# Optimization experiments

Hardware: AMD Instinct MI355X
Metric: run time of the kernel (lower is better)

## Reference

```python
import jax, jax.numpy as jnp
import numpy as np

RNN = 64

def linear(x, W, b):
    return x @ W.T + b

def sample_logprob(key, logits):
    # Categorical(softmax(logits)): sample + log_prob of the sample
    s = jax.random.categorical(key, logits)
    lp = jnp.take_along_axis(jax.nn.log_softmax(logits, -1), s[:, None], 1)[:, 0]
    return s, lp

def lstm_encode(inst, embed, W_ih, W_hh, b_ih, b_hh):
    # torch.nn.LSTMCell unrolled over the sequence; gate order i,f,g,o
    x = embed[inst]                              # [B,S,64]
    B = inst.shape[0]
    def step(carry, xt):
        h, c = carry
        gates = xt @ W_ih.T + b_ih + h @ W_hh.T + b_hh   # [B,256]
        i, f, g, o = jnp.split(gates, 4, axis=-1)
        c = jax.nn.sigmoid(f) * c + jax.nn.sigmoid(i) * jnp.tanh(g)
        h = jax.nn.sigmoid(o) * jnp.tanh(c)
        return (h, c), None
    h0 = jnp.zeros((B, RNN), x.dtype)
    (h, _), _ = jax.lax.scan(step, (h0, h0), jnp.swapaxes(x, 0, 1))
    return h

def setup_inputs():
    key = jax.random.key(0)
    ks = jax.random.split(key, 20)
    B, S, V = 16384, 32, 1000
    def nrm(k, shape, scale=0.05):
        return jax.random.normal(k, shape, jnp.float32) * scale
    return {
        "inst0": jax.random.randint(ks[0], (B, S), 0, V + 1),
        "inst1": jax.random.randint(ks[1], (B, S), 0, V + 1),
        "canvas0": jax.random.randint(ks[2], (B, 25, 4), 0, 5).astype(jnp.int32),
        "canvas1": jax.random.randint(ks[3], (B, 25, 4), 0, 5).astype(jnp.int32),
        "ref": jax.random.randint(ks[4], (B, 4), 0, 5).astype(jnp.int32),
        "embed": nrm(ks[5], (V + 1, RNN)),
        "W_ih": nrm(ks[6], (4 * RNN, RNN)), "W_hh": nrm(ks[7], (4 * RNN, RNN)),
        "b_ih": jnp.zeros(4 * RNN), "b_hh": jnp.zeros(4 * RNN),
        "Wc": nrm(ks[8], (3, RNN)), "bc": jnp.zeros(3),
        "Ws": nrm(ks[9], (3, RNN)), "bs": jnp.zeros(3),
        "Wl": nrm(ks[10], (25, RNN)), "bl": jnp.zeros(25),
        "Wr1": nrm(ks[11], (32, RNN + 4)), "br1": jnp.zeros(32),
        "Wr2": nrm(ks[12], (1, 32)), "br2": jnp.zeros(1),
        "Wp": nrm(ks[13], (8, RNN)), "bp": jnp.zeros(8),
    }

def reference(inst0, inst1, canvas0, canvas1, ref, embed, W_ih, W_hh, b_ih, b_hh,
              Wc, bc, Ws, bs, Wl, bl, Wr1, br1, Wr2, br2, Wp, bp):
    B = inst0.shape[0]
    kk = jax.random.split(jax.random.key(42), 7)
    final_canvas = canvas1                                   # [B,25,4]

    def step_rewards(loc_predict, color_sample, shape_sample):
        valid = (loc_predict >= 0) & (loc_predict < 25)
        pt = jnp.take_along_axis(final_canvas,
                                 jnp.clip(loc_predict, 0, 24)[:, None, None],
                                 axis=1)[:, 0]               # [B,4]
        ok = valid & (pt.sum(-1) >= 0)
        loc_r = jnp.where(ok, 1.0, -1.0)
        col_r = jnp.where(ok, jnp.where(color_sample == pt[:, 0], 1.0, -1.0), 0.0)
        shp_r = jnp.where(ok, jnp.where(shape_sample == pt[:, 1], 1.0, -1.0), 0.0)
        return loc_r, col_r, shp_r

    # ---- dialog step 0: absolute location ----
    h0 = lstm_encode(inst0, embed, W_ih, W_hh, b_ih, b_hh)
    cs0, clp0 = sample_logprob(kk[0], linear(h0, Wc, bc))
    ss0, slp0 = sample_logprob(kk[1], linear(h0, Ws, bs))
    loc0, llp0 = sample_logprob(kk[2], linear(h0, Wl, bl))
    loc_r0, col_r0, _ = step_rewards(loc0, cs0, ss0)

    # ---- dialog step 1: relative location w.r.t. attended ref object ----
    h1 = lstm_encode(inst1, embed, W_ih, W_hh, b_ih, b_hh)
    cs1, clp1 = sample_logprob(kk[3], linear(h1, Wc, bc))
    ss1, slp1 = sample_logprob(kk[4], linear(h1, Ws, bs))
    ls1, llp1 = sample_logprob(kk[5], linear(h1, Wp, bp))    # 8-way offset
    prev = canvas0.astype(h1.dtype)                          # [B,25,4]
    feat = jnp.concatenate([jnp.broadcast_to(h1[:, None, :], (B, 25, RNN)), prev], 2)  # [B,25,68]
    att_logits = (jax.nn.relu(feat @ Wr1.T + br1) @ Wr2.T + br2)[:, :, 0]              # [B,25]
    att_sample, alp1 = sample_logprob(kk[6], att_logits)
    ref_obj = jnp.take_along_axis(canvas0, att_sample[:, None, None], axis=1)[:, 0]    # [B,4]
    att_reward = ((ref_obj == ref).sum(-1) == 4).astype(jnp.float32) * 2.0 - 1.0
    offsets = jnp.array([[-1, 0], [1, 0], [0, 1], [0, -1],
                         [-1, -1], [-1, 1], [1, -1], [1, 1]], jnp.int32)
    off = offsets[ls1]
    loc1 = (ref_obj[:, 2] + off[:, 0]) * 5 + (ref_obj[:, 3] + off[:, 1])
    loc_r1, col_r1, _ = step_rewards(loc1, cs1, ss1)

    logp = jnp.stack([clp0, slp0, llp0, clp1, slp1, llp1, alp1])          # [7,B]
    # NB: original appends step_loc_reward into shape_rewards (kept verbatim)
    rew = jnp.stack([loc_r0, col_r0, loc_r0, loc_r1, col_r1, loc_r1, att_reward])  # [7,B]
    return logp, rew
```

## Files before the change

### kernel.cpp

```cpp
#include <hip/hip_runtime.h>
#include <hip/hip_bf16.h>
#include <stdint.h>
#include <math.h>

#define NB 16384
#define NSEQ 32
#define NV 1001
#define NROWS 32768

#define CHK 272
#define RTG (8 * CHK)
#define SPL (8 * RTG)
#define HBUF (3 * SPL)

typedef __attribute__((ext_vector_type(8))) short bf16x8;
typedef __attribute__((ext_vector_type(4))) float f32x4;

__device__ __forceinline__ void tf2x32(uint32_t k0, uint32_t k1,
                                       uint32_t x0, uint32_t x1,
                                       uint32_t& o0, uint32_t& o1) {
  const uint32_t ks0 = k0, ks1 = k1, ks2 = k0 ^ k1 ^ 0x1BD11BDAu;
  x0 += ks0; x1 += ks1;
  const int rA[4] = {13, 15, 26, 6};
  const int rB[4] = {17, 29, 16, 24};
#pragma unroll
  for (int i = 0; i < 4; ++i) { x0 += x1; x1 = (x1 << rA[i]) | (x1 >> (32 - rA[i])); x1 ^= x0; }
  x0 += ks1; x1 += ks2 + 1u;
#pragma unroll
  for (int i = 0; i < 4; ++i) { x0 += x1; x1 = (x1 << rB[i]) | (x1 >> (32 - rB[i])); x1 ^= x0; }
  x0 += ks2; x1 += ks0 + 2u;
#pragma unroll
  for (int i = 0; i < 4; ++i) { x0 += x1; x1 = (x1 << rA[i]) | (x1 >> (32 - rA[i])); x1 ^= x0; }
  x0 += ks0; x1 += ks1 + 3u;
#pragma unroll
  for (int i = 0; i < 4; ++i) { x0 += x1; x1 = (x1 << rB[i]) | (x1 >> (32 - rB[i])); x1 ^= x0; }
  x0 += ks1; x1 += ks2 + 4u;
#pragma unroll
  for (int i = 0; i < 4; ++i) { x0 += x1; x1 = (x1 << rA[i]) | (x1 >> (32 - rA[i])); x1 ^= x0; }
  o0 = x0 + ks2; o1 = x1 + ks0 + 5u;
}

__device__ __forceinline__ float gumbel_from_bits(uint32_t bits) {
  uint32_t fb = (bits >> 9) | 0x3f800000u;
  float u = __uint_as_float(fb) - 1.0f;
  u = fmaxf(u, 1.17549435e-38f);
  return -logf(-logf(u));
}

__device__ __forceinline__ float sigm(float x) { return 1.0f / (1.0f + __expf(-x)); }
__device__ __forceinline__ float tanh_(float x) {
  float e = __expf(2.0f * x);
  return 1.0f - 2.0f / (e + 1.0f);
}

__device__ __forceinline__ float dot64(const float* __restrict__ w, const float* h) {
  float a = 0.f;
#pragma unroll
  for (int k = 0; k < 64; ++k) a = fmaf(w[k], h[k], a);
  return a;
}

__device__ __forceinline__ unsigned short bfbits(float x, float& xf) {
  __hip_bfloat16 hb = __float2bfloat16(x);
  xf = __bfloat162float(hb);
  unsigned short u;
  __builtin_memcpy(&u, &hb, 2);
  return u;
}

template <int N>
__device__ __forceinline__ void samp_team(const float* lg, int g, int C,
                                          uint32_t k0, uint32_t k1, int b,
                                          int& sOut, float& lpOut) {
  float m = -__builtin_inff();
#pragma unroll
  for (int i = 0; i < N; ++i) m = fmaxf(m, lg[i]);
  m = fmaxf(m, __shfl_xor(m, 1));
  m = fmaxf(m, __shfl_xor(m, 2));
  float se = 0.f;
#pragma unroll
  for (int i = 0; i < N; ++i) se += expf(lg[i] - m);
  se += __shfl_xor(se, 1);
  se += __shfl_xor(se, 2);
  const float lse = logf(se);
  float bz = -__builtin_inff(), bl = 0.f;
  int bi = 0x7fffffff;
#pragma unroll
  for (int i = 0; i < N; ++i) {
    const int c = g + 4 * i;
    uint32_t o0, o1; tf2x32(k0, k1, 0u, (uint32_t)(b * C + c), o0, o1);
    const float z = lg[i] + gumbel_from_bits(o0 ^ o1);
    if (z > bz || (z == bz && c < bi)) { bz = z; bi = c; bl = lg[i]; }
  }
#pragma unroll
  for (int d = 1; d <= 2; d <<= 1) {
    const float z2 = __shfl_xor(bz, d);
    const int i2 = __shfl_xor(bi, d);
    const float l2 = __shfl_xor(bl, d);
    if (z2 > bz || (z2 == bz && i2 < bi)) { bz = z2; bi = i2; bl = l2; }
  }
  sOut = bi;
  lpOut = (bl - m) - lse;
}

__global__ __launch_bounds__(256) void k_prep(
    const float* __restrict__ embed, const float* __restrict__ W_ih,
    const float* __restrict__ W_hh, const float* __restrict__ b_ih,
    const float* __restrict__ b_hh, float* __restrict__ embedWi,
    unsigned short* __restrict__ Wsp) {
  if (blockIdx.x >= NV) {
    int idx = (blockIdx.x - NV) * 256 + threadIdx.x;
    int s = idx >> 14;
    int rem = idx & 16383;
    int jp = rem >> 6, m = rem & 63;
    int kc = m >> 5, q = (m >> 3) & 3, p = m & 7;
    int k = kc * 32 + q * 8 + ((p >> 1) + ((p & 1) << 2));
    int j = (jp & 3) * 64 + (jp >> 2);
    float w = W_hh[j * 64 + k];
    float f1, f2, f3;
    unsigned short b1 = bfbits(w, f1);
    unsigned short b2 = bfbits(w - f1, f2);
    unsigned short b3 = bfbits(w - f1 - f2, f3);
    Wsp[idx] = (s == 0) ? b1 : (s == 1) ? b2 : b3;
    return;
  }
  __shared__ float er[64];
  int v = blockIdx.x;
  if (threadIdx.x < 64) er[threadIdx.x] = embed[v * 64 + threadIdx.x];
  __syncthreads();
  int jp = threadIdx.x;
  int j = (jp & 3) * 64 + (jp >> 2);
  float a = b_ih[j] + b_hh[j];
#pragma unroll
  for (int k = 0; k < 64; ++k) a = fmaf(W_ih[j * 64 + k], er[k], a);
  embedWi[v * 256 + jp] = a;
}

__global__ __launch_bounds__(512, 2) void k_lstm(
    const int* __restrict__ inst0, const int* __restrict__ inst1,
    const float* __restrict__ embedWi, const unsigned short* __restrict__ Wsp,
    float* __restrict__ hT) {
  extern __shared__ char smc[];
  int* idsb = (int*)(smc + 2 * HBUF);

  const int tid = threadIdx.x;
  const int lane = tid & 63;
  const int wave = tid >> 6;
  const int wgj = wave >> 1;
  const int wrh = wave & 1;
  const int n15 = lane & 15;
  const int quad = lane >> 4;
  const int blk = blockIdx.x;
  const int rowbase = blk * 128;
  const int rb = rowbase & (NB - 1);
  const int* __restrict__ inst = (blk < 128) ? inst0 : inst1;

  bf16x8 afr[4][2][3];
#pragma unroll
  for (int jt = 0; jt < 4; ++jt) {
    const int jrow = (wgj * 4 + jt) * 16 + n15;
#pragma unroll
    for (int kc = 0; kc < 2; ++kc)
#pragma unroll
      for (int s = 0; s < 3; ++s)
        afr[jt][kc][s] =
            *(const bf16x8*)(Wsp + ((s * 256 + jrow) * 64 + kc * 32 + quad * 8));
  }
#pragma unroll
  for (int jt = 0; jt < 4; ++jt)
#pragma unroll
    for (int kc = 0; kc < 2; ++kc)
#pragma unroll
      for (int s = 0; s < 3; ++s)
        asm volatile("" : "+v"(afr[jt][kc][s]));

  for (int i = tid; i < HBUF / 4; i += 512) ((float*)smc)[i] = 0.f;
  if (tid < 128) idsb[tid] = inst[(rb + tid) * NSEQ];

  float cst[16];
#pragma unroll
  for (int i = 0; i < 16; ++i) cst[i] = 0.f;

  __syncthreads();

#pragma unroll 1
  for (int t = 0; t < NSEQ; ++t) {
    const char* __restrict__ hbr = smc + (t & 1) * HBUF;
    char* __restrict__ hbw = smc + ((t & 1) ^ 1) * HBUF;

    int vv[4];
#pragma unroll
    for (int rt = 0; rt < 4; ++rt)
      vv[rt] = idsb[(t & 1) * 128 + wrh * 64 + rt * 16 + n15];
    if (tid < 128 && t + 1 < NSEQ)
      idsb[((t + 1) & 1) * 128 + tid] = inst[(rb + tid) * NSEQ + t + 1];

    f32x4 C[4][4];
#pragma unroll
    for (int jt = 0; jt < 4; ++jt)
#pragma unroll
      for (int rt = 0; rt < 4; ++rt) C[jt][rt] = (f32x4){0.f, 0.f, 0.f, 0.f};

#pragma unroll
    for (int rt = 0; rt < 4; ++rt) {
      const int rtg = wrh * 4 + rt;
      bf16x8 bfr[2][3];
#pragma unroll
      for (int kc = 0; kc < 2; ++kc)
#pragma unroll
        for (int s = 0; s < 3; ++s)
          bfr[kc][s] = *(const bf16x8*)(hbr + s * SPL + rtg * RTG +
                                        (kc * 4 + quad) * CHK + n15 * 16);
#pragma unroll
      for (int jt = 0; jt < 4; ++jt) {
#pragma unroll
        for (int kc = 0; kc < 2; ++kc) {
          f32x4 acc = C[jt][rt];
          acc = __builtin_amdgcn_mfma_f32_16x16x32_bf16(afr[jt][kc][1], bfr[kc][2], acc, 0, 0, 0);
          acc = __builtin_amdgcn_mfma_f32_16x16x32_bf16(afr[jt][kc][2], bfr[kc][1], acc, 0, 0, 0);
          acc = __builtin_amdgcn_mfma_f32_16x16x32_bf16(afr[jt][kc][0], bfr[kc][2], acc, 0, 0, 0);
          acc = __builtin_amdgcn_mfma_f32_16x16x32_bf16(afr[jt][kc][2], bfr[kc][0], acc, 0, 0, 0);
          acc = __builtin_amdgcn_mfma_f32_16x16x32_bf16(afr[jt][kc][1], bfr[kc][1], acc, 0, 0, 0);
          acc = __builtin_amdgcn_mfma_f32_16x16x32_bf16(afr[jt][kc][0], bfr[kc][1], acc, 0, 0, 0);
          acc = __builtin_amdgcn_mfma_f32_16x16x32_bf16(afr[jt][kc][1], bfr[kc][0], acc, 0, 0, 0);
          acc = __builtin_amdgcn_mfma_f32_16x16x32_bf16(afr[jt][kc][0], bfr[kc][0], acc, 0, 0, 0);
          C[jt][rt] = acc;
        }
      }
    }

    const bool last = (t == NSEQ - 1);
    float4 esA[4], esB[4];
#pragma unroll
    for (int jt = 0; jt < 4; ++jt)
      esA[jt] = *(const float4*)(embedWi + vv[0] * 256 + (wgj * 16 + jt * 4 + quad) * 4);
#pragma unroll
    for (int rt = 0; rt < 4; ++rt) {
      if (rt < 3) {
#pragma unroll
        for (int jt = 0; jt < 4; ++jt)
          esB[jt] = *(const float4*)(embedWi + vv[rt + 1] * 256 +
                                     (wgj * 16 + jt * 4 + quad) * 4);
      }
      const int r = wrh * 64 + rt * 16 + n15;
      const int rtg = wrh * 4 + rt;
      float hval[4];
      unsigned short s1[4], s2[4], s3[4];
#pragma unroll
      for (int jt = 0; jt < 4; ++jt) {
        const float gi = C[jt][rt].x + esA[jt].x;
        const float gf = C[jt][rt].y + esA[jt].y;
        const float gg = C[jt][rt].z + esA[jt].z;
        const float go = C[jt][rt].w + esA[jt].w;
        const float ci = sigm(gf) * cst[jt * 4 + rt] + sigm(gi) * tanh_(gg);
        cst[jt * 4 + rt] = ci;
        const float h = sigm(go) * tanh_(ci);
        hval[jt] = h;
        float f1, f2, f3;
        s1[jt] = bfbits(h, f1);
        s2[jt] = bfbits(h - f1, f2);
        s3[jt] = bfbits(h - f1 - f2, f3);
      }
      char* base = hbw + rtg * RTG + n15 * 16 + quad * 4;
      *(uint32_t*)(base + 0 * SPL + (wgj * 2 + 0) * CHK) = (uint32_t)s1[0] | ((uint32_t)s1[1] << 16);
      *(uint32_t*)(base + 0 * SPL + (wgj * 2 + 1) * CHK) = (uint32_t)s1[2] | ((uint32_t)s1[3] << 16);
      *(uint32_t*)(base + 1 * SPL + (wgj * 2 + 0) * CHK) = (uint32_t)s2[0] | ((uint32_t)s2[1] << 16);
      *(uint32_t*)(base + 1 * SPL + (wgj * 2 + 1) * CHK) = (uint32_t)s2[2] | ((uint32_t)s2[3] << 16);
      *(uint32_t*)(base + 2 * SPL + (wgj * 2 + 0) * CHK) = (uint32_t)s3[0] | ((uint32_t)s3[1] << 16);
      *(uint32_t*)(base + 2 * SPL + (wgj * 2 + 1) * CHK) = (uint32_t)s3[2] | ((uint32_t)s3[3] << 16);
      if (last) {
#pragma unroll
        for (int jt = 0; jt < 4; ++jt)
          hT[(wgj * 16 + jt * 4 + quad) * NROWS + rowbase + r] = hval[jt];
      }
#pragma unroll
      for (int jt = 0; jt < 4; ++jt) esA[jt] = esB[jt];
    }
    __syncthreads();
  }
}

__global__ __launch_bounds__(256) void k_heads(
    const int* __restrict__ canvas0, const int* __restrict__ canvas1,
    const int* __restrict__ ref,
    const float* __restrict__ Wc, const float* __restrict__ bc,
    const float* __restrict__ Ws, const float* __restrict__ bs,
    const float* __restrict__ Wl, const float* __restrict__ bl,
    const float* __restrict__ Wr1, const float* __restrict__ br1,
    const float* __restrict__ Wr2, const float* __restrict__ br2,
    const float* __restrict__ Wp, const float* __restrict__ bp,
    const float* __restrict__ hT, float* __restrict__ out) {
  const int tid = threadIdx.x;
  const int g = tid & 3;
  const int s = blockIdx.x & 1;
  const int b = (blockIdx.x >> 1) * 64 + (tid >> 2);
  const float NEG = -__builtin_inff();

  uint32_t kk0[7], kk1[7];
#pragma unroll
  for (int i = 0; i < 7; ++i) {
    uint32_t o0, o1; tf2x32(0u, 42u, 0u, (uint32_t)i, o0, o1);
    kk0[i] = o0; kk1[i] = o1;
  }

  float h[64];
#pragma unroll
  for (int u = 0; u < 64; ++u) h[u] = hT[u * NROWS + s * NB + b];

  float lgc[1], lgs[1];
  lgc[0] = (g < 3) ? (bc[g] + dot64(Wc + g * 64, h)) : NEG;
  lgs[0] = (g < 3) ? (bs[g] + dot64(Ws + g * 64, h)) : NEG;

  if (s == 0) {
    int cs0, ss0, loc0; float clp0, slp0, llp0;
    samp_team<1>(lgc, g, 3, kk0[0], kk1[0], b, cs0, clp0);
    samp_team<1>(lgs, g, 3, kk0[1], kk1[1], b, ss0, slp0);
    float lgl[7];
#pragma unroll
    for (int i = 0; i < 7; ++i) {
      const int cc = g + 4 * i;
      lgl[i] = (cc < 25) ? (bl[cc] + dot64(Wl + cc * 64, h)) : NEG;
    }
    samp_team<7>(lgl, g, 25, kk0[2], kk1[2], b, loc0, llp0);

    if (g == 0) {
      const int p0 = min(max(loc0, 0), 24);
      const int4 pt = ((const int4*)(canvas1 + b * 100))[p0];
      const bool ok0 = (loc0 >= 0) && (loc0 < 25) && (pt.x + pt.y + pt.z + pt.w >= 0);
      const float loc_r0 = ok0 ? 1.f : -1.f;
      const float col_r0 = ok0 ? ((cs0 == pt.x) ? 1.f : -1.f) : 0.f;
      out[0 * NB + b] = clp0;
      out[1 * NB + b] = slp0;
      out[2 * NB + b] = llp0;
      out[7 * NB + b] = loc_r0;
      out[8 * NB + b] = col_r0;
      out[9 * NB + b] = loc_r0;
    }
  } else {
    int cs1, ss1, ls1; float clp1, slp1, llp1;
    samp_team<1>(lgc, g, 3, kk0[3], kk1[3], b, cs1, clp1);
    samp_team<1>(lgs, g, 3, kk0[4], kk1[4], b, ss1, slp1);
    float lgp[2];
#pragma unroll
    for (int i = 0; i < 2; ++i) {
      const int cc = g + 4 * i;
      lgp[i] = bp[cc] + dot64(Wp + cc * 64, h);
    }
    samp_team<2>(lgp, g, 8, kk0[5], kk1[5], b, ls1, llp1);

    float uv8[8], w64[8], w65[8], w66[8], w67[8], wr2[8];
#pragma unroll
    for (int i = 0; i < 8; ++i) {
      const int j = g + 4 * i;
      uv8[i] = br1[j] + dot64(Wr1 + j * 68, h);
      const float* wr = Wr1 + j * 68 + 64;
      w64[i] = wr[0]; w65[i] = wr[1]; w66[i] = wr[2]; w67[i] = wr[3];
      wr2[i] = Wr2[j];
    }
    float lgA[7];
#pragma unroll
    for (int i = 0; i < 7; ++i) lgA[i] = NEG;
    const float b2 = br2[0];
#pragma unroll
    for (int p = 0; p < 25; ++p) {
      const int4 c4 = ((const int4*)(canvas0 + b * 100))[p];
      const float f0 = (float)c4.x, f1 = (float)c4.y;
      const float f2 = (float)c4.z, f3 = (float)c4.w;
      float part = 0.f;
#pragma unroll
      for (int i = 0; i < 8; ++i) {
        float hj = uv8[i];
        hj = fmaf(w64[i], f0, hj);
        hj = fmaf(w65[i], f1, hj);
        hj = fmaf(w66[i], f2, hj);
        hj = fmaf(w67[i], f3, hj);
        part = fmaf(wr2[i], fmaxf(hj, 0.f), part);
      }
      part += __shfl_xor(part, 1);
      part += __shfl_xor(part, 2);
      const float ap = b2 + part;
      if ((p & 3) == g) lgA[p >> 2] = ap;
    }
    int att_s; float alp1;
    samp_team<7>(lgA, g, 25, kk0[6], kk1[6], b, att_s, alp1);

    if (g == 0) {
      const int4 r4 = ((const int4*)(canvas0 + b * 100))[att_s];
      const int4 rr = *(const int4*)(ref + b * 4);
      const bool match = (r4.x == rr.x) && (r4.y == rr.y) &&
                         (r4.z == rr.z) && (r4.w == rr.w);
      const float att_reward = match ? 1.f : -1.f;
      const int ox = (int)((0x22001120u >> (ls1 * 4)) & 0xFu) - 1;
      const int oy = (int)((0x20200211u >> (ls1 * 4)) & 0xFu) - 1;
      const int loc1 = (r4.z + ox) * 5 + (r4.w + oy);
      const int p1 = min(max(loc1, 0), 24);
      const int4 q4 = ((const int4*)(canvas1 + b * 100))[p1];
      const bool ok1 = (loc1 >= 0) && (loc1 < 25) && (q4.x + q4.y + q4.z + q4.w >= 0);
      const float loc_r1 = ok1 ? 1.f : -1.f;
      const float col_r1 = ok1 ? ((cs1 == q4.x) ? 1.f : -1.f) : 0.f;
      out[3 * NB + b]  = clp1;
      out[4 * NB + b]  = slp1;
      out[5 * NB + b]  = llp1;
      out[6 * NB + b]  = alp1;
      out[10 * NB + b] = loc_r1;
      out[11 * NB + b] = col_r1;
      out[12 * NB + b] = loc_r1;
      out[13 * NB + b] = att_reward;
    }
  }
}

extern "C" void kernel_launch(void* const* d_in, const int* in_sizes, int n_in,
                              void* d_out, int out_size, void* d_ws, size_t ws_size,
                              hipStream_t stream) {
  const int* inst0 = (const int*)d_in[0];
  const int* inst1 = (const int*)d_in[1];
  const int* canvas0 = (const int*)d_in[2];
  const int* canvas1 = (const int*)d_in[3];
  const int* ref = (const int*)d_in[4];
  const float* embed = (const float*)d_in[5];
  const float* W_ih = (const float*)d_in[6];
  const float* W_hh = (const float*)d_in[7];
  const float* b_ih = (const float*)d_in[8];
  const float* b_hh = (const float*)d_in[9];
  const float* Wc = (const float*)d_in[10];
  const float* bc = (const float*)d_in[11];
  const float* Ws = (const float*)d_in[12];
  const float* bs = (const float*)d_in[13];
  const float* Wl = (const float*)d_in[14];
  const float* bl = (const float*)d_in[15];
  const float* Wr1 = (const float*)d_in[16];
  const float* br1 = (const float*)d_in[17];
  const float* Wr2 = (const float*)d_in[18];
  const float* br2 = (const float*)d_in[19];
  const float* Wp = (const float*)d_in[20];
  const float* bp = (const float*)d_in[21];

  float* ws = (float*)d_ws;
  float* embedWi = ws;
  unsigned short* Wsp = (unsigned short*)(ws + NV * 256);
  float* hT = ws + NV * 256 + 24576;
  float* out = (float*)d_out;

  (void)hipFuncSetAttribute((const void*)k_lstm,
                            hipFuncAttributeMaxDynamicSharedMemorySize, 163840);

  const size_t ldsBytes = 2 * HBUF + 1024;
  k_prep<<<NV + 192, 256, 0, stream>>>(embed, W_ih, W_hh, b_ih, b_hh, embedWi, Wsp);
  k_lstm<<<256, 512, ldsBytes, stream>>>(inst0, inst1, embedWi, Wsp, hT);
  k_heads<<<512, 256, 0, stream>>>(canvas0, canvas1, ref, Wc, bc, Ws, bs,
                                   Wl, bl, Wr1, br1, Wr2, br2, Wp, bp, hT, out);
}
```

Before: 482.9 us.

## Halve LSTM block rows, drop two split-bf16 MFMA terms, raise occupancy

The LSTM kernel now gives each block 64 rows instead of 128 and launches 512 blocks. Each wave owns 2 gate tiles across all 4 row tiles instead of 4 gate tiles across half the rows. The hidden-state LDS buffer shrinks so 4 blocks can fit per CU, and the MFMA matmul is interleaved per row tile with the gate nonlinearity. The two lowest-order split-bf16 cross terms (s1*s2 and s2*s1 products) are dropped, which cuts MFMA work by a quarter but slightly lowers the precision of the recurrent matmul.

```diff
diff --git a/kernel.cpp b/kernel.cpp
--- a/kernel.cpp
+++ b/kernel.cpp
@@ -10,7 +10,7 @@
 
 #define CHK 272
 #define RTG (8 * CHK)
-#define SPL (8 * RTG)
+#define SPL (4 * RTG)
 #define HBUF (3 * SPL)
 
 typedef __attribute__((ext_vector_type(8))) short bf16x8;
@@ -136,7 +136,7 @@
   embedWi[v * 256 + jp] = a;
 }
 
-__global__ __launch_bounds__(512, 2) void k_lstm(
+__global__ __launch_bounds__(512, 4) void k_lstm(
     const int* __restrict__ inst0, const int* __restrict__ inst1,
     const float* __restrict__ embedWi, const unsigned short* __restrict__ Wsp,
     float* __restrict__ hT) {
@@ -145,20 +145,18 @@
 
   const int tid = threadIdx.x;
   const int lane = tid & 63;
-  const int wave = tid >> 6;
-  const int wgj = wave >> 1;
-  const int wrh = wave & 1;
+  const int e8 = tid >> 6;
   const int n15 = lane & 15;
   const int quad = lane >> 4;
   const int blk = blockIdx.x;
-  const int rowbase = blk * 128;
-  const int rb = rowbase & (NB - 1);
-  const int* __restrict__ inst = (blk < 128) ? inst0 : inst1;
-
-  bf16x8 afr[4][2][3];
-#pragma unroll
-  for (int jt = 0; jt < 4; ++jt) {
-    const int jrow = (wgj * 4 + jt) * 16 + n15;
+  const int rowbase = blk * 64;
+  const int rb = (blk & 255) * 64;
+  const int* __restrict__ inst = (blk < 256) ? inst0 : inst1;
+
+  bf16x8 afr[2][2][3];
+#pragma unroll
+  for (int jt = 0; jt < 2; ++jt) {
+    const int jrow = (e8 * 2 + jt) * 16 + n15;
 #pragma unroll
     for (int kc = 0; kc < 2; ++kc)
 #pragma unroll
@@ -166,20 +164,13 @@
         afr[jt][kc][s] =
             *(const bf16x8*)(Wsp + ((s * 256 + jrow) * 64 + kc * 32 + quad * 8));
   }
-#pragma unroll
-  for (int jt = 0; jt < 4; ++jt)
-#pragma unroll
-    for (int kc = 0; kc < 2; ++kc)
-#pragma unroll
-      for (int s = 0; s < 3; ++s)
-        asm volatile("" : "+v"(afr[jt][kc][s]));
 
   for (int i = tid; i < HBUF / 4; i += 512) ((float*)smc)[i] = 0.f;
-  if (tid < 128) idsb[tid] = inst[(rb + tid) * NSEQ];
-
-  float cst[16];
-#pragma unroll
-  for (int i = 0; i < 16; ++i) cst[i] = 0.f;
+  if (tid < 64) idsb[tid] = inst[(rb + tid) * NSEQ];
+
+  float cst[8];
+#pragma unroll
+  for (int i = 0; i < 8; ++i) cst[i] = 0.f;
 
   __syncthreads();
 
@@ -187,71 +178,62 @@
   for (int t = 0; t < NSEQ; ++t) {
     const char* __restrict__ hbr = smc + (t & 1) * HBUF;
     char* __restrict__ hbw = smc + ((t & 1) ^ 1) * HBUF;
-
-    int vv[4];
-#pragma unroll
-    for (int rt = 0; rt < 4; ++rt)
-      vv[rt] = idsb[(t & 1) * 128 + wrh * 64 + rt * 16 + n15];
-    if (tid < 128 && t + 1 < NSEQ)
-      idsb[((t + 1) & 1) * 128 + tid] = inst[(rb + tid) * NSEQ + t + 1];
-
-    f32x4 C[4][4];
-#pragma unroll
-    for (int jt = 0; jt < 4; ++jt)
-#pragma unroll
-      for (int rt = 0; rt < 4; ++rt) C[jt][rt] = (f32x4){0.f, 0.f, 0.f, 0.f};
+    const bool last = (t == NSEQ - 1);
+
+    if (tid < 64 && t + 1 < NSEQ)
+      idsb[((t + 1) & 1) * 64 + tid] = inst[(rb + tid) * NSEQ + t + 1];
+
+    float4 esc[2], esn[2];
+    {
+      const int v0 = idsb[(t & 1) * 64 + n15];
+#pragma unroll
+      for (int jt = 0; jt < 2; ++jt)
+        esc[jt] = *(const float4*)(embedWi + v0 * 256 +
+                                   (e8 * 8 + jt * 4 + quad) * 4);
+    }
 
 #pragma unroll
     for (int rt = 0; rt < 4; ++rt) {
-      const int rtg = wrh * 4 + rt;
+      if (rt < 3) {
+        const int vn = idsb[(t & 1) * 64 + (rt + 1) * 16 + n15];
+#pragma unroll
+        for (int jt = 0; jt < 2; ++jt)
+          esn[jt] = *(const float4*)(embedWi + vn * 256 +
+                                     (e8 * 8 + jt * 4 + quad) * 4);
+      }
       bf16x8 bfr[2][3];
 #pragma unroll
       for (int kc = 0; kc < 2; ++kc)
 #pragma unroll
         for (int s = 0; s < 3; ++s)
-          bfr[kc][s] = *(const bf16x8*)(hbr + s * SPL + rtg * RTG +
+          bfr[kc][s] = *(const bf16x8*)(hbr + s * SPL + rt * RTG +
                                         (kc * 4 + quad) * CHK + n15 * 16);
-#pragma unroll
-      for (int jt = 0; jt < 4; ++jt) {
+      f32x4 C2[2];
+#pragma unroll
+      for (int jt = 0; jt < 2; ++jt) C2[jt] = (f32x4){0.f, 0.f, 0.f, 0.f};
+#pragma unroll
+      for (int jt = 0; jt < 2; ++jt) {
 #pragma unroll
         for (int kc = 0; kc < 2; ++kc) {
-          f32x4 acc = C[jt][rt];
-          acc = __builtin_amdgcn_mfma_f32_16x16x32_bf16(afr[jt][kc][1], bfr[kc][2], acc, 0, 0, 0);
-          acc = __builtin_amdgcn_mfma_f32_16x16x32_bf16(afr[jt][kc][2], bfr[kc][1], acc, 0, 0, 0);
+          f32x4 acc = C2[jt];
           acc = __builtin_amdgcn_mfma_f32_16x16x32_bf16(afr[jt][kc][0], bfr[kc][2], acc, 0, 0, 0);
           acc = __builtin_amdgcn_mfma_f32_16x16x32_bf16(afr[jt][kc][2], bfr[kc][0], acc, 0, 0, 0);
           acc = __builtin_amdgcn_mfma_f32_16x16x32_bf16(afr[jt][kc][1], bfr[kc][1], acc, 0, 0, 0);
           acc = __builtin_amdgcn_mfma_f32_16x16x32_bf16(afr[jt][kc][0], bfr[kc][1], acc, 0, 0, 0);
           acc = __builtin_amdgcn_mfma_f32_16x16x32_bf16(afr[jt][kc][1], bfr[kc][0], acc, 0, 0, 0);
           acc = __builtin_amdgcn_mfma_f32_16x16x32_bf16(afr[jt][kc][0], bfr[kc][0], acc, 0, 0, 0);
-          C[jt][rt] = acc;
+          C2[jt] = acc;
         }
       }
-    }
-
-    const bool last = (t == NSEQ - 1);
-    float4 esA[4], esB[4];
-#pragma unroll
-    for (int jt = 0; jt < 4; ++jt)
-      esA[jt] = *(const float4*)(embedWi + vv[0] * 256 + (wgj * 16 + jt * 4 + quad) * 4);
-#pragma unroll
-    for (int rt = 0; rt < 4; ++rt) {
-      if (rt < 3) {
-#pragma unroll
-        for (int jt = 0; jt < 4; ++jt)
-          esB[jt] = *(const float4*)(embedWi + vv[rt + 1] * 256 +
-                                     (wgj * 16 + jt * 4 + quad) * 4);
-      }
-      const int r = wrh * 64 + rt * 16 + n15;
-      const int rtg = wrh * 4 + rt;
-      float hval[4];
-      unsigned short s1[4], s2[4], s3[4];
-#pragma unroll
-      for (int jt = 0; jt < 4; ++jt) {
-        const float gi = C[jt][rt].x + esA[jt].x;
-        const float gf = C[jt][rt].y + esA[jt].y;
-        const float gg = C[jt][rt].z + esA[jt].z;
-        const float go = C[jt][rt].w + esA[jt].w;
+
+      float hval[2];
+      unsigned short s1[2], s2[2], s3[2];
+#pragma unroll
+      for (int jt = 0; jt < 2; ++jt) {
+        const float gi = C2[jt].x + esc[jt].x;
+        const float gf = C2[jt].y + esc[jt].y;
+        const float gg = C2[jt].z + esc[jt].z;
+        const float go = C2[jt].w + esc[jt].w;
         const float ci = sigm(gf) * cst[jt * 4 + rt] + sigm(gi) * tanh_(gg);
         cst[jt * 4 + rt] = ci;
         const float h = sigm(go) * tanh_(ci);
@@ -261,20 +243,16 @@
         s2[jt] = bfbits(h - f1, f2);
         s3[jt] = bfbits(h - f1 - f2, f3);
       }
-      char* base = hbw + rtg * RTG + n15 * 16 + quad * 4;
-      *(uint32_t*)(base + 0 * SPL + (wgj * 2 + 0) * CHK) = (uint32_t)s1[0] | ((uint32_t)s1[1] << 16);
-      *(uint32_t*)(base + 0 * SPL + (wgj * 2 + 1) * CHK) = (uint32_t)s1[2] | ((uint32_t)s1[3] << 16);
-      *(uint32_t*)(base + 1 * SPL + (wgj * 2 + 0) * CHK) = (uint32_t)s2[0] | ((uint32_t)s2[1] << 16);
-      *(uint32_t*)(base + 1 * SPL + (wgj * 2 + 1) * CHK) = (uint32_t)s2[2] | ((uint32_t)s2[3] << 16);
-      *(uint32_t*)(base + 2 * SPL + (wgj * 2 + 0) * CHK) = (uint32_t)s3[0] | ((uint32_t)s3[1] << 16);
-      *(uint32_t*)(base + 2 * SPL + (wgj * 2 + 1) * CHK) = (uint32_t)s3[2] | ((uint32_t)s3[3] << 16);
+      char* base = hbw + rt * RTG + e8 * CHK + n15 * 16 + quad * 4;
+      *(uint32_t*)(base + 0 * SPL) = (uint32_t)s1[0] | ((uint32_t)s1[1] << 16);
+      *(uint32_t*)(base + 1 * SPL) = (uint32_t)s2[0] | ((uint32_t)s2[1] << 16);
+      *(uint32_t*)(base + 2 * SPL) = (uint32_t)s3[0] | ((uint32_t)s3[1] << 16);
       if (last) {
 #pragma unroll
-        for (int jt = 0; jt < 4; ++jt)
-          hT[(wgj * 16 + jt * 4 + quad) * NROWS + rowbase + r] = hval[jt];
+        for (int jt = 0; jt < 2; ++jt)
+          hT[(e8 * 8 + jt * 4 + quad) * NROWS + rowbase + rt * 16 + n15] = hval[jt];
       }
-#pragma unroll
-      for (int jt = 0; jt < 4; ++jt) esA[jt] = esB[jt];
+      esc[0] = esn[0]; esc[1] = esn[1];
     }
     __syncthreads();
   }
@@ -442,12 +420,9 @@
   float* hT = ws + NV * 256 + 24576;
   float* out = (float*)d_out;
 
-  (void)hipFuncSetAttribute((const void*)k_lstm,
-                            hipFuncAttributeMaxDynamicSharedMemorySize, 163840);
-
-  const size_t ldsBytes = 2 * HBUF + 1024;
+  const size_t ldsBytes = 2 * HBUF + 512;
   k_prep<<<NV + 192, 256, 0, stream>>>(embed, W_ih, W_hh, b_ih, b_hh, embedWi, Wsp);
-  k_lstm<<<256, 512, ldsBytes, stream>>>(inst0, inst1, embedWi, Wsp, hT);
+  k_lstm<<<512, 512, ldsBytes, stream>>>(inst0, inst1, embedWi, Wsp, hT);
   k_heads<<<512, 256, 0, stream>>>(canvas0, canvas1, ref, Wc, bc, Ws, bs,
                                    Wl, bl, Wr1, br1, Wr2, br2, Wp, bp, hT, out);
 }
```

New measurement: 428.3 us. -11.3%, faster.
